# Kernel optimization log

Hardware: AMD Instinct MI355X
Metric: run time of the kernel (lower is better)

Reference implementation:

```python
import jax, jax.numpy as jnp
import numpy as np

B, C, D = 512, 100000, 512
MARGIN = 0.5  # ArcFace-style additive angular margin


def setup_inputs() -> dict:
    key = jax.random.key(0)
    k1, k2, k3 = jax.random.split(key, 3)
    embeddings = jax.random.normal(k1, (B, D), dtype=jnp.float32)
    labels = jax.random.randint(k2, (B,), 0, C, dtype=jnp.int32)
    weight = 0.01 * jax.random.normal(k3, (C, D), dtype=jnp.float32)  # torch.normal(0, 0.01, (C, D))
    return {"embeddings": embeddings, "labels": labels, "weight": weight}


def _l2_normalize(x, eps=1e-12):
    return x / jnp.maximum(jnp.linalg.norm(x, axis=-1, keepdims=True), eps)


def reference(embeddings, labels, weight):
    cos_m = jnp.cos(MARGIN)
    sin_m = jnp.sin(MARGIN)

    e = _l2_normalize(embeddings)          # (B, D)
    w = _l2_normalize(weight)              # (C, D)
    logits = jnp.clip(jnp.einsum('bd,cd->bc', e, w), -1.0, 1.0)  # (B, C) cosines

    bsz, ncls = logits.shape
    rows = jnp.arange(bsz)
    cos_t = logits[rows, labels]                                   # (B,) cos(theta_y)
    sin_t = jnp.sqrt(jnp.clip(1.0 - cos_t * cos_t, 0.0, None))     # sin(theta_y)
    cos_tm = cos_t * cos_m - sin_t * sin_m                         # cos(theta_y + m)
    sin_tm = sin_t * cos_m + cos_t * sin_m                         # sin(theta_y + m)

    # non-target class indices per row, ascending, skipping the target: (B, C-1)
    base = jnp.arange(ncls - 1)[None, :]
    nt_idx = base + (base >= labels[:, None]).astype(base.dtype)

    # margin_softmax: logits2 = cos(theta_j) - cos(theta_y + m) over non-target j
    nt_logits = jnp.take_along_axis(logits, nt_idx, axis=1)       # (B, C-1)
    logits2 = nt_logits - cos_tm[:, None]

    # no_grad block: weight_m is unit-norm point at angle theta_y+m from e,
    # so ||w_j - w_m||^2 = 2 - 2 <w_j, w_m>  (avoids materializing (B, C, D)).
    w_y = w[labels]                                                # (B, D)
    w_m = (-sin_m * e + sin_tm[:, None] * w_y) / sin_t[:, None]    # (B, D), unit norm
    sim = jnp.einsum('bd,cd->bc', w_m, w)                          # (B, C)
    nt_sim = jnp.take_along_axis(sim, nt_idx, axis=1)              # (B, C-1)
    diff_weight_norm = jax.lax.stop_gradient(
        jnp.sqrt(jnp.clip(2.0 - 2.0 * nt_sim, 0.0, None)))         # (B, C-1)

    e_logits = jnp.sum(jnp.exp(logits2 / diff_weight_norm), axis=1)  # (B,)
    return jnp.mean(jnp.log1p(e_logits))
```

## Files before the change

kernel.cpp:

```cpp
#include <hip/hip_runtime.h>
#include <hip/hip_fp8.h>
#include <math.h>

#define B_SZ 512
#define C_SZ 100000
#define D_SZ 512

#define BN 128
#define NTILES 782
#define MT 8
#define NBLK (NTILES * MT)
#define KSTEPS 8
#define DEPTH 2

typedef __attribute__((ext_vector_type(4))) float f32x4;
typedef __attribute__((ext_vector_type(16))) float f32x16;
typedef __attribute__((ext_vector_type(4))) int i32x4;
typedef __attribute__((ext_vector_type(8))) int i32x8;

#define UNITY_SCALE 0x7F7F7F7F

__device__ __forceinline__ void gload_lds16(const void* gptr, void* lptr) {
  __builtin_amdgcn_global_load_lds(
      (const __attribute__((address_space(1))) void*)gptr,
      (__attribute__((address_space(3))) void*)lptr,
      16, 0, 0);
}

__device__ __forceinline__ unsigned char f2fp8(float x) {
  __hip_fp8_e4m3 h(x);
  return (unsigned char)h.__x;
}
__device__ __forceinline__ float fp82f(unsigned int u) {
  __hip_fp8_e4m3 h;
  h.__x = (unsigned char)u;
  return (float)h;
}
__device__ __forceinline__ unsigned int pack4f8(float a, float b, float c, float d) {
  return (unsigned int)f2fp8(a) | ((unsigned int)f2fp8(b) << 8) |
         ((unsigned int)f2fp8(c) << 16) | ((unsigned int)f2fp8(d) << 24);
}

__device__ __forceinline__ i32x8 ld_frag(const unsigned char* base, int frag, int l) {
  i32x4 lo = *(const i32x4*)(base + frag * 2048 + l * 16);
  i32x4 hg = *(const i32x4*)(base + frag * 2048 + 1024 + l * 16);
  return __builtin_shufflevector(lo, hg, 0, 1, 2, 3, 4, 5, 6, 7);
}
__device__ __forceinline__ i32x8 ld_a(const unsigned char* p) {
  i32x4 lo = *(const i32x4*)(p);
  i32x4 hg = *(const i32x4*)(p + 1024);
  return __builtin_shufflevector(lo, hg, 0, 1, 2, 3, 4, 5, 6, 7);
}

__global__ __launch_bounds__(256) void k_norm_w(const float* __restrict__ w,
                                                unsigned char* __restrict__ w8) {
  const int row = blockIdx.x * 4 + (threadIdx.x >> 6);
  const int lane = threadIdx.x & 63;
  const float4* wr = (const float4*)(w + (size_t)row * D_SZ);
  float4 v0 = wr[lane];
  float4 v1 = wr[64 + lane];
  float ss = v0.x*v0.x + v0.y*v0.y + v0.z*v0.z + v0.w*v0.w
           + v1.x*v1.x + v1.y*v1.y + v1.z*v1.z + v1.w*v1.w;
  #pragma unroll
  for (int o = 32; o; o >>= 1) ss += __shfl_xor(ss, o, 64);
  const float rn = __builtin_amdgcn_rsqf(fmaxf(ss, 1e-24f));
  unsigned int* out = (unsigned int*)(w8 + (size_t)row * D_SZ);
  out[lane] = pack4f8(v0.x * rn, v0.y * rn, v0.z * rn, v0.w * rn);
  out[64 + lane] = pack4f8(v1.x * rn, v1.y * rn, v1.z * rn, v1.w * rn);
}

__global__ __launch_bounds__(64) void k_prep(const float* __restrict__ e,
                                             const int* __restrict__ labels,
                                             const unsigned char* __restrict__ w8,
                                             unsigned char* __restrict__ A8f,
                                             float4* __restrict__ params) {
  const int b = blockIdx.x;
  const int lane = threadIdx.x;
  const float4* er = (const float4*)(e + (size_t)b * D_SZ);
  float4 v0 = er[lane], v1 = er[64 + lane];
  float ss = v0.x*v0.x + v0.y*v0.y + v0.z*v0.z + v0.w*v0.w
           + v1.x*v1.x + v1.y*v1.y + v1.z*v1.z + v1.w*v1.w;
  #pragma unroll
  for (int o = 32; o; o >>= 1) ss += __shfl_xor(ss, o, 64);
  const float rn = __builtin_amdgcn_rsqf(fmaxf(ss, 1e-24f));
  v0.x *= rn; v0.y *= rn; v0.z *= rn; v0.w *= rn;
  v1.x *= rn; v1.y *= rn; v1.z *= rn; v1.w *= rn;

  const unsigned int ue0 = pack4f8(v0.x, v0.y, v0.z, v0.w);
  const unsigned int ue1 = pack4f8(v1.x, v1.y, v1.z, v1.w);

  const int lab = labels[b];
  const unsigned int* wr = (const unsigned int*)(w8 + (size_t)lab * D_SZ);
  const unsigned int w0 = wr[lane], w1 = wr[64 + lane];

  const int re = 2 * b;
  const int frag = re >> 5;
  const int rife = re & 31;
  const int wk = (4 * lane) & 63;
  const int ks = lane >> 4;
  const int sbits = (((wk >> 5) & 1) << 5) | (((wk >> 4) & 1) << 6);
  const int byteo = wk & 15;
  unsigned char* fb = A8f + (size_t)frag * 16384;
  unsigned char* pe = fb + (rife | sbits) * 16 + byteo;
  unsigned char* pw = fb + ((rife + 1) | sbits) * 16 + byteo;
  *(unsigned int*)(pe + ks * 2048) = ue0;
  *(unsigned int*)(pe + (ks + 4) * 2048) = ue1;
  *(unsigned int*)(pw + ks * 2048) = w0;
  *(unsigned int*)(pw + (ks + 4) * 2048) = w1;

  float d = v0.x * fp82f(w0 & 255) + v0.y * fp82f((w0 >> 8) & 255)
          + v0.z * fp82f((w0 >> 16) & 255) + v0.w * fp82f(w0 >> 24)
          + v1.x * fp82f(w1 & 255) + v1.y * fp82f((w1 >> 8) & 255)
          + v1.z * fp82f((w1 >> 16) & 255) + v1.w * fp82f(w1 >> 24);
  #pragma unroll
  for (int o = 32; o; o >>= 1) d += __shfl_xor(d, o, 64);

  if (lane == 0) {
    const float cos_m = 0.877582561890372716f;
    const float sin_m = 0.479425538604203000f;
    float cos_t = fminf(fmaxf(d, -1.0f), 1.0f);
    float sin_t = sqrtf(fmaxf(1.0f - cos_t * cos_t, 0.0f));
    float cos_tm = cos_t * cos_m - sin_t * sin_m;
    float sin_tm = sin_t * cos_m + cos_t * sin_m;
    float inv_st = 1.0f / fmaxf(sin_t, 1e-20f);
    params[b] = make_float4(cos_tm, sin_m * inv_st, sin_tm * inv_st, 0.0f);
  }
}

__device__ __forceinline__ float termf(float de, float dwy, float4 p, bool kill) {
  float c = fminf(fmaxf(de, -1.0f), 1.0f);
  float s = p.z * dwy - p.y * de;
  float x = fmaxf(fmaf(-2.0f, s, 2.0f), 1e-20f);
  float t = (c - p.x) * __builtin_amdgcn_rsqf(x);
  float r = __expf(t);
  return kill ? 0.0f : r;
}

__global__ __launch_bounds__(512, 6) void k_gemm(const unsigned char* __restrict__ A8f,
                                                 const unsigned char* __restrict__ W8,
                                                 const float4* __restrict__ params,
                                                 const int* __restrict__ labels,
                                                 float* __restrict__ part) {
  __shared__ __align__(32) unsigned char Bt[DEPTH][BN * 64];
  __shared__ float ered[64];
  __shared__ float4 pl[64];
  __shared__ int ll[64];

  const int bid = blockIdx.x;
  const int p = (bid & 7) * (NBLK / 8) + (bid >> 3);
  const int nt = p >> 3, mt = p & 7;
  const int t = threadIdx.x;
  const int w = t >> 6, l = t & 63;
  const int n0 = nt * BN;
  const int b0 = mt * 64;

  if (t < 64) {
    ered[t] = 0.0f;
    pl[t] = params[b0 + t];
    ll[t] = labels[b0 + t];
  }

  const int kpart = ((t >> 5) & 1) * 32 + ((t >> 6) & 1) * 16;
  int brow_s = n0 + (t >> 7) * 32 + (t & 31);
  if (brow_s >= C_SZ) brow_s = C_SZ - 1;
  const int boffs = brow_s * D_SZ + kpart;

  const unsigned char* afb =
      A8f + (size_t)(mt * 4 + (w & 3)) * 16384 + l * 16;

  f32x16 accA = {}, accB = {};
  const int fA = w & 3;
  const int fB0 = (w >> 2) * 2;
  const int hi = l >> 5;

#define STAGE(d, ts)                                                        \
  gload_lds16(W8 + (size_t)(boffs + (ts) * 64), (void*)(Bt[d] + t * 16))

  STAGE(0, 0);
  STAGE(1, 1);
  asm volatile("s_waitcnt vmcnt(1) lgkmcnt(0)" ::: "memory");
  __builtin_amdgcn_s_barrier();

  #pragma unroll
  for (int s = 0; s < KSTEPS; ++s) {
    const int d = s & 1;
    i32x8 av = ld_a(afb + s * 2048);
    i32x8 bv = ld_frag(Bt[d], fB0, l);
    __builtin_amdgcn_s_setprio(1);
    accA = __builtin_amdgcn_mfma_scale_f32_32x32x64_f8f6f4(
        av, bv, accA, 0, 0, 0, UNITY_SCALE, 0, UNITY_SCALE);
    bv = ld_frag(Bt[d], fB0 + 1, l);
    accB = __builtin_amdgcn_mfma_scale_f32_32x32x64_f8f6f4(
        av, bv, accB, 0, 0, 0, UNITY_SCALE, 0, UNITY_SCALE);
    __builtin_amdgcn_s_setprio(0);
    if (s < KSTEPS - 1) {
      asm volatile("s_waitcnt vmcnt(0)" ::: "memory");
      __builtin_amdgcn_s_barrier();
      if (s + 2 < KSTEPS)
        STAGE(d, s + 2);
    }
  }
#undef STAGE

  #pragma unroll
  for (int rp = 0; rp < 8; ++rp) {
    const int r = 2 * rp;
    const int lb = fA * 16 + (rp & 1) + 4 * (rp >> 1) + 2 * hi;
    float4 pp = pl[lb];
    int lab = ll[lb];
    int j0 = n0 + fB0 * 32 + (l & 31);
    int j1 = j0 + 32;
    float s = termf(accA[r], accA[r + 1], pp, (j0 >= C_SZ) || (j0 == lab))
            + termf(accB[r], accB[r + 1], pp, (j1 >= C_SZ) || (j1 == lab));
    #pragma unroll
    for (int o = 1; o < 32; o <<= 1) s += __shfl_xor(s, o, 64);
    if ((l & 31) == 0) atomicAdd(&ered[lb], s);
  }
  __syncthreads();
  if (t < 64) part[(size_t)(b0 + t) * NTILES + nt] = ered[t];
}

__global__ __launch_bounds__(256) void k_rowsum(const float* __restrict__ part,
                                                float* __restrict__ rowsum) {
  const int b = blockIdx.x;
  float s = 0.0f;
  for (int i = threadIdx.x; i < NTILES; i += 256) s += part[(size_t)b * NTILES + i];
  #pragma unroll
  for (int o = 32; o; o >>= 1) s += __shfl_xor(s, o, 64);
  __shared__ float red[4];
  if ((threadIdx.x & 63) == 0) red[threadIdx.x >> 6] = s;
  __syncthreads();
  if (threadIdx.x == 0)
    rowsum[b] = log1pf(red[0] + red[1] + red[2] + red[3]);
}

__global__ __launch_bounds__(512) void k_final(const float* __restrict__ rowsum,
                                               float* __restrict__ out) {
  const int b = threadIdx.x;
  float v = rowsum[b];
  __shared__ float red[512];
  red[b] = v;
  __syncthreads();
  #pragma unroll
  for (int o = 256; o; o >>= 1) {
    if (b < o) red[b] += red[b + o];
    __syncthreads();
  }
  if (b == 0) out[0] = red[0] / (float)B_SZ;
}

extern "C" void kernel_launch(void* const* d_in, const int* in_sizes, int n_in,
                              void* d_out, int out_size, void* d_ws, size_t ws_size,
                              hipStream_t stream) {
  const float* emb = (const float*)d_in[0];
  const int* labels = (const int*)d_in[1];
  const float* w = (const float*)d_in[2];

  char* ws = (char*)d_ws;
  unsigned char* w8 = (unsigned char*)ws;
  size_t off = (size_t)C_SZ * D_SZ;
  unsigned char* A8f = (unsigned char*)(ws + off);
  off += (size_t)2 * B_SZ * D_SZ;
  float4* params = (float4*)(ws + off);
  off += (size_t)B_SZ * 16;
  float* part = (float*)(ws + off);
  off += (size_t)B_SZ * NTILES * 4;
  float* rowsum = (float*)(ws + off);
  off += (size_t)B_SZ * 4;

  k_norm_w<<<dim3(C_SZ / 4), dim3(256), 0, stream>>>(w, w8);
  k_prep<<<dim3(B_SZ), dim3(64), 0, stream>>>(emb, labels, w8, A8f, params);
  k_gemm<<<dim3(NBLK), dim3(512), 0, stream>>>(A8f, w8, params, labels, part);
  k_rowsum<<<dim3(B_SZ), dim3(256), 0, stream>>>(part, rowsum);
  k_final<<<dim3(1), dim3(512), 0, stream>>>(rowsum, (float*)d_out);
}
```

Before: 135.4 us.

## Store normalized weights in MFMA fragment layout and load B directly from global

The weight normalization kernel now writes the fp8 weights in the pre-swizzled 32-row MFMA fragment layout. The GEMM then reads B operands straight from global memory into registers instead of staging them through double-buffered LDS with global_load_lds and barriers. Params and labels are read from global in the epilogue rather than from shared memory. This removes LDS traffic and per-step barriers, but it loses the software pipeline. Global latency is exposed each k-step (the loop is no longer unrolled), and B data is reloaded by each wave that uses it instead of being shared.

```diff
diff --git a/kernel.cpp b/kernel.cpp
--- a/kernel.cpp
+++ b/kernel.cpp
@@ -11,7 +11,7 @@
 #define MT 8
 #define NBLK (NTILES * MT)
 #define KSTEPS 8
-#define DEPTH 2
+#define NGRP 3125
 
 typedef __attribute__((ext_vector_type(4))) float f32x4;
 typedef __attribute__((ext_vector_type(16))) float f32x16;
@@ -20,13 +20,6 @@
 
 #define UNITY_SCALE 0x7F7F7F7F
 
-__device__ __forceinline__ void gload_lds16(const void* gptr, void* lptr) {
-  __builtin_amdgcn_global_load_lds(
-      (const __attribute__((address_space(1))) void*)gptr,
-      (__attribute__((address_space(3))) void*)lptr,
-      16, 0, 0);
-}
-
 __device__ __forceinline__ unsigned char f2fp8(float x) {
   __hip_fp8_e4m3 h(x);
   return (unsigned char)h.__x;
@@ -41,11 +34,6 @@
          ((unsigned int)f2fp8(c) << 16) | ((unsigned int)f2fp8(d) << 24);
 }
 
-__device__ __forceinline__ i32x8 ld_frag(const unsigned char* base, int frag, int l) {
-  i32x4 lo = *(const i32x4*)(base + frag * 2048 + l * 16);
-  i32x4 hg = *(const i32x4*)(base + frag * 2048 + 1024 + l * 16);
-  return __builtin_shufflevector(lo, hg, 0, 1, 2, 3, 4, 5, 6, 7);
-}
 __device__ __forceinline__ i32x8 ld_a(const unsigned char* p) {
   i32x4 lo = *(const i32x4*)(p);
   i32x4 hg = *(const i32x4*)(p + 1024);
@@ -53,7 +41,7 @@
 }
 
 __global__ __launch_bounds__(256) void k_norm_w(const float* __restrict__ w,
-                                                unsigned char* __restrict__ w8) {
+                                                unsigned char* __restrict__ w8f) {
   const int row = blockIdx.x * 4 + (threadIdx.x >> 6);
   const int lane = threadIdx.x & 63;
   const float4* wr = (const float4*)(w + (size_t)row * D_SZ);
@@ -64,14 +52,22 @@
   #pragma unroll
   for (int o = 32; o; o >>= 1) ss += __shfl_xor(ss, o, 64);
   const float rn = __builtin_amdgcn_rsqf(fmaxf(ss, 1e-24f));
-  unsigned int* out = (unsigned int*)(w8 + (size_t)row * D_SZ);
-  out[lane] = pack4f8(v0.x * rn, v0.y * rn, v0.z * rn, v0.w * rn);
-  out[64 + lane] = pack4f8(v1.x * rn, v1.y * rn, v1.z * rn, v1.w * rn);
+
+  const int g = row >> 5, rif = row & 31;
+  const int wk = (4 * lane) & 63;
+  const int ks = lane >> 4;
+  const int sbits = (((wk >> 5) & 1) << 5) | (((wk >> 4) & 1) << 6);
+  const int byteo = wk & 15;
+  unsigned char* base = w8f + (size_t)g * 16384 + (rif | sbits) * 16 + byteo;
+  *(unsigned int*)(base + ks * 2048) =
+      pack4f8(v0.x * rn, v0.y * rn, v0.z * rn, v0.w * rn);
+  *(unsigned int*)(base + (ks + 4) * 2048) =
+      pack4f8(v1.x * rn, v1.y * rn, v1.z * rn, v1.w * rn);
 }
 
 __global__ __launch_bounds__(64) void k_prep(const float* __restrict__ e,
                                              const int* __restrict__ labels,
-                                             const unsigned char* __restrict__ w8,
+                                             const unsigned char* __restrict__ w8f,
                                              unsigned char* __restrict__ A8f,
                                              float4* __restrict__ params) {
   const int b = blockIdx.x;
@@ -89,17 +85,20 @@
   const unsigned int ue0 = pack4f8(v0.x, v0.y, v0.z, v0.w);
   const unsigned int ue1 = pack4f8(v1.x, v1.y, v1.z, v1.w);
 
-  const int lab = labels[b];
-  const unsigned int* wr = (const unsigned int*)(w8 + (size_t)lab * D_SZ);
-  const unsigned int w0 = wr[lane], w1 = wr[64 + lane];
-
-  const int re = 2 * b;
-  const int frag = re >> 5;
-  const int rife = re & 31;
   const int wk = (4 * lane) & 63;
   const int ks = lane >> 4;
   const int sbits = (((wk >> 5) & 1) << 5) | (((wk >> 4) & 1) << 6);
   const int byteo = wk & 15;
+
+  const int lab = labels[b];
+  const unsigned char* wbase =
+      w8f + (size_t)(lab >> 5) * 16384 + ((lab & 31) | sbits) * 16 + byteo;
+  const unsigned int w0 = *(const unsigned int*)(wbase + ks * 2048);
+  const unsigned int w1 = *(const unsigned int*)(wbase + (ks + 4) * 2048);
+
+  const int re = 2 * b;
+  const int frag = re >> 5;
+  const int rife = re & 31;
   unsigned char* fb = A8f + (size_t)frag * 16384;
   unsigned char* pe = fb + (rife | sbits) * 16 + byteo;
   unsigned char* pw = fb + ((rife + 1) | sbits) * 16 + byteo;
@@ -137,14 +136,11 @@
 }
 
 __global__ __launch_bounds__(512, 6) void k_gemm(const unsigned char* __restrict__ A8f,
-                                                 const unsigned char* __restrict__ W8,
+                                                 const unsigned char* __restrict__ W8f,
                                                  const float4* __restrict__ params,
                                                  const int* __restrict__ labels,
                                                  float* __restrict__ part) {
-  __shared__ __align__(32) unsigned char Bt[DEPTH][BN * 64];
   __shared__ float ered[64];
-  __shared__ float4 pl[64];
-  __shared__ int ll[64];
 
   const int bid = blockIdx.x;
   const int p = (bid & 7) * (NBLK / 8) + (bid >> 3);
@@ -154,60 +150,45 @@
   const int n0 = nt * BN;
   const int b0 = mt * 64;
 
-  if (t < 64) {
-    ered[t] = 0.0f;
-    pl[t] = params[b0 + t];
-    ll[t] = labels[b0 + t];
-  }
-
-  const int kpart = ((t >> 5) & 1) * 32 + ((t >> 6) & 1) * 16;
-  int brow_s = n0 + (t >> 7) * 32 + (t & 31);
-  if (brow_s >= C_SZ) brow_s = C_SZ - 1;
-  const int boffs = brow_s * D_SZ + kpart;
+  if (t < 64) ered[t] = 0.0f;
 
   const unsigned char* afb =
       A8f + (size_t)(mt * 4 + (w & 3)) * 16384 + l * 16;
 
+  const int fB0 = (w >> 2) * 2;
+  int gB0 = nt * 4 + fB0;
+  int gB1 = gB0 + 1;
+  if (gB0 > NGRP - 1) gB0 = NGRP - 1;
+  if (gB1 > NGRP - 1) gB1 = NGRP - 1;
+  const unsigned char* bfb0 = W8f + (size_t)gB0 * 16384 + l * 16;
+  const unsigned char* bfb1 = W8f + (size_t)gB1 * 16384 + l * 16;
+
   f32x16 accA = {}, accB = {};
   const int fA = w & 3;
-  const int fB0 = (w >> 2) * 2;
   const int hi = l >> 5;
 
-#define STAGE(d, ts)                                                        \
-  gload_lds16(W8 + (size_t)(boffs + (ts) * 64), (void*)(Bt[d] + t * 16))
-
-  STAGE(0, 0);
-  STAGE(1, 1);
-  asm volatile("s_waitcnt vmcnt(1) lgkmcnt(0)" ::: "memory");
-  __builtin_amdgcn_s_barrier();
-
-  #pragma unroll
+  #pragma unroll 1
   for (int s = 0; s < KSTEPS; ++s) {
-    const int d = s & 1;
     i32x8 av = ld_a(afb + s * 2048);
-    i32x8 bv = ld_frag(Bt[d], fB0, l);
+    i32x8 bv0 = ld_a(bfb0 + s * 2048);
+    i32x8 bv1 = ld_a(bfb1 + s * 2048);
     __builtin_amdgcn_s_setprio(1);
     accA = __builtin_amdgcn_mfma_scale_f32_32x32x64_f8f6f4(
-        av, bv, accA, 0, 0, 0, UNITY_SCALE, 0, UNITY_SCALE);
-    bv = ld_frag(Bt[d], fB0 + 1, l);
+        av, bv0, accA, 0, 0, 0, UNITY_SCALE, 0, UNITY_SCALE);
     accB = __builtin_amdgcn_mfma_scale_f32_32x32x64_f8f6f4(
-        av, bv, accB, 0, 0, 0, UNITY_SCALE, 0, UNITY_SCALE);
+        av, bv1, accB, 0, 0, 0, UNITY_SCALE, 0, UNITY_SCALE);
     __builtin_amdgcn_s_setprio(0);
-    if (s < KSTEPS - 1) {
-      asm volatile("s_waitcnt vmcnt(0)" ::: "memory");
-      __builtin_amdgcn_s_barrier();
-      if (s + 2 < KSTEPS)
-        STAGE(d, s + 2);
-    }
-  }
-#undef STAGE
+  }
+
+  __syncthreads();
 
   #pragma unroll
   for (int rp = 0; rp < 8; ++rp) {
     const int r = 2 * rp;
     const int lb = fA * 16 + (rp & 1) + 4 * (rp >> 1) + 2 * hi;
-    float4 pp = pl[lb];
-    int lab = ll[lb];
+    const int gb = b0 + lb;
+    float4 pp = params[gb];
+    int lab = labels[gb];
     int j0 = n0 + fB0 * 32 + (l & 31);
     int j1 = j0 + 32;
     float s = termf(accA[r], accA[r + 1], pp, (j0 >= C_SZ) || (j0 == lab))
@@ -257,10 +238,10 @@
   const float* w = (const float*)d_in[2];
 
   char* ws = (char*)d_ws;
-  unsigned char* w8 = (unsigned char*)ws;
-  size_t off = (size_t)C_SZ * D_SZ;
+  unsigned char* w8f = (unsigned char*)ws;
+  size_t off = (size_t)NGRP * 16384;
   unsigned char* A8f = (unsigned char*)(ws + off);
-  off += (size_t)2 * B_SZ * D_SZ;
+  off += (size_t)32 * 16384;
   float4* params = (float4*)(ws + off);
   off += (size_t)B_SZ * 16;
   float* part = (float*)(ws + off);
@@ -268,9 +249,9 @@
   float* rowsum = (float*)(ws + off);
   off += (size_t)B_SZ * 4;
 
-  k_norm_w<<<dim3(C_SZ / 4), dim3(256), 0, stream>>>(w, w8);
-  k_prep<<<dim3(B_SZ), dim3(64), 0, stream>>>(emb, labels, w8, A8f, params);
-  k_gemm<<<dim3(NBLK), dim3(512), 0, stream>>>(A8f, w8, params, labels, part);
+  k_norm_w<<<dim3(C_SZ / 4), dim3(256), 0, stream>>>(w, w8f);
+  k_prep<<<dim3(B_SZ), dim3(64), 0, stream>>>(emb, labels, w8f, A8f, params);
+  k_gemm<<<dim3(NBLK), dim3(512), 0, stream>>>(A8f, w8f, params, labels, part);
   k_rowsum<<<dim3(B_SZ), dim3(256), 0, stream>>>(part, rowsum);
   k_final<<<dim3(1), dim3(512), 0, stream>>>(rowsum, (float*)d_out);
 }
```

After: 141.5 us. +4.5%, slower.
